# Kernel tuning notes

Measured on AMD Instinct MI355X. Metric: run time of the kernel, lower is better.

The kernel has to match this reference:

```python
import jax, jax.numpy as jnp
import numpy as np

B, L, HID = 512, 128, 384
N_LABELS, N_SLOTS = 32, 128


def setup_inputs() -> dict:
    key = jax.random.key(0)
    ks = jax.random.split(key, 16)

    def g(k, shape, scale):
        return jax.random.normal(k, shape, dtype=jnp.float32) * scale

    sent_lens = jax.random.randint(ks[0], (B,), 1, L + 1)
    mask = (jnp.arange(L)[None, :] < sent_lens[:, None]).astype(jnp.float32)[..., None]
    # zero out padded token positions to mimic the ragged original
    H = g(ks[1], (B, L, HID), 1.0) * mask
    c_slot_cont = g(ks[2], (B, L, HID), 1.0) * mask
    c_inte = g(ks[3], (B, HID), 1.0)
    s = 1.0 / np.sqrt(HID)
    return {
        "H": H,
        "c_slot_cont": c_slot_cont,
        "c_inte": c_inte,
        "W0": g(ks[4], (HID, HID), s),
        "W1": g(ks[5], (HID, HID), s),
        "W2": g(ks[6], (HID, HID), s),
        "W3": g(ks[7], (HID, HID), s),
        "W4": g(ks[8], (HID, HID), s),
        "b4": g(ks[9], (HID,), s),
        "W5": g(ks[10], (HID, 1), s),
        "V_SF": g(ks[11], (HID, HID), s),
        "W_inte": g(ks[12], (HID, N_LABELS), s),
        "W_slot": g(ks[13], (2 * HID, N_SLOTS), s),
        "sent_lens": sent_lens,
        "iteration_num": 3,
    }


def reference(H, c_slot_cont, c_inte, W0, W1, W2, W3, W4, b4, W5, V_SF,
              W_inte, W_slot, sent_lens, iteration_num):
    Ld = H.shape[1]
    mask = jnp.arange(Ld)[None, :] < sent_lens[:, None]          # [B, L] bool
    maskf = mask[..., None].astype(H.dtype)                       # [B, L, 1]
    neg_inf = jnp.finfo(H.dtype).min

    def sf_fusion(x, y):
        # SF_FusionLayer (dropout off / eval); inner loop runs once since nth=2
        x0 = jnp.tanh(x)
        y0 = jnp.tanh(y)
        f = jax.nn.sigmoid(jnp.tanh(x0 @ W0 + y0 @ W1) @ W2)
        x2 = f * x0 + x
        y2 = (1.0 - f) * y0 + y
        return f * x2 + (1.0 - f) * y2

    def id_fusion(x, y):
        # ID_FusionLayer; softmax over token dim, masked per sentence
        x0 = jnp.tanh(x)
        y0 = jnp.tanh(y)
        rates = ((x @ W3 + y @ W4 + b4) @ W5)[..., 0]             # [B, L]
        rates = jnp.where(mask, rates, neg_inf)
        alphas = jax.nn.softmax(rates, axis=1)[..., None]         # [B, L, 1]
        x2 = alphas * x0 + x
        y2 = (1.0 - alphas) * y0 + y
        return alphas * x2 + (1.0 - alphas) * y2

    r_inte = c_inte                                               # [B, HID]
    r_slot = c_slot_cont
    for _ in range(iteration_num):
        f_slot = sf_fusion(c_slot_cont, r_inte[:, None, :])       # [B, L, HID]
        f_slot = jnp.sum((f_slot @ V_SF) * maskf, axis=1)         # [B, HID]
        r_slot = f_slot[:, None, :] * c_slot_cont                 # [B, L, HID]
        f_inte = jnp.sum(id_fusion(r_slot, H) * maskf, axis=1)    # [B, HID]
        r_inte = f_inte + c_inte

    intent_output = r_inte @ W_inte                               # [B, n_labels]
    slot_output = jnp.concatenate([H, r_slot], axis=-1) @ W_slot  # [B, L, n_slots]
    return intent_output, slot_output
```

## Files before the change

### kernel.cpp

```cpp
#include <hip/hip_runtime.h>
#include <math.h>

#define HID 384
#define SLEN 128
#define NB 512
#define MTOK (NB*SLEN)
#define NLAB 32
#define NSLOT 128
#define GPITCH 72

typedef _Float16 h8 __attribute__((ext_vector_type(8)));
typedef _Float16 h4v __attribute__((ext_vector_type(4)));
typedef __bf16   b8 __attribute__((ext_vector_type(8)));
typedef float    f4 __attribute__((ext_vector_type(4)));

__device__ __forceinline__ float sane(float x){
  return __builtin_isfinite(x) ? x : 0.f;
}
__device__ __forceinline__ float clampf(float x, float lo, float hi){
  return fminf(hi, fmaxf(lo, x));
}
__device__ __forceinline__ float fast_rcp(float x){
  return __builtin_amdgcn_rcpf(x);
}
__device__ __forceinline__ float fast_tanh(float x){
  x = clampf(x, -15.f, 15.f);
  float e = __expf(2.f * x);
  return (e - 1.f) * fast_rcp(e + 1.f);
}
__device__ __forceinline__ float sigmoid_c(float x){
  x = clampf(x, -60.f, 60.f);
  return fast_rcp(1.f + __expf(-x));
}
__device__ __forceinline__ void split16(float x, _Float16* h, _Float16* l){
  _Float16 hh = (_Float16)x; *h = hh; *l = (_Float16)(x - (float)hh);
}
__device__ __forceinline__ h8 ldh(const _Float16* p){ return *reinterpret_cast<const h8*>(p); }
__device__ __forceinline__ b8 ldb(const __bf16* p){ return *reinterpret_cast<const b8*>(p); }
__device__ __forceinline__ f4 mfma16h(h8 a, h8 b, f4 c){
  return __builtin_amdgcn_mfma_f32_16x16x32_f16(a, b, c, 0, 0, 0);
}
__device__ __forceinline__ f4 mfma16b(b8 a, b8 b, f4 c){
  return __builtin_amdgcn_mfma_f32_16x16x32_bf16(a, b, c, 0, 0, 0);
}
__device__ __forceinline__ void bar_lds(){
  asm volatile("s_waitcnt lgkmcnt(0)" ::: "memory");
  __builtin_amdgcn_s_barrier();
}


__global__ void k_lens(const int* __restrict__ raw, int* __restrict__ lensN){
  const int b = threadIdx.x;
  __shared__ int is64;
  if (b == 0) is64 = (raw[1] == 0) ? 1 : 0;
  __syncthreads();
  int v = is64 ? raw[2 * b] : raw[b];
  v = v < 0 ? 0 : (v > SLEN ? SLEN : v);
  lensN[b] = v;
}

__global__ void k_wsplit16(const float* __restrict__ in, _Float16* __restrict__ outh,
                           _Float16* __restrict__ outl, int R, int C){
  int idx = blockIdx.x * blockDim.x + threadIdx.x;
  if (idx < R * C){
    int r = idx / C, c = idx - r * C;
    float v = sane(in[idx]);
    _Float16 h = (_Float16)v;
    outh[(size_t)c * R + r] = h;
    outl[(size_t)c * R + r] = (_Float16)(v - (float)h);
  }
}

__global__ void k_wsplitbf(const float* __restrict__ in, __bf16* __restrict__ outh,
                           __bf16* __restrict__ outl, int R, int C){
  int idx = blockIdx.x * blockDim.x + threadIdx.x;
  if (idx < R * C){
    int r = idx / C, c = idx - r * C;
    float v = sane(in[idx]);
    __bf16 h = (__bf16)v;
    outh[(size_t)c * R + r] = h;
    outl[(size_t)c * R + r] = (__bf16)(v - (float)h);
  }
}

__global__ void k_transpose32(const float* __restrict__ in, float* __restrict__ out,
                              int R, int C){
  int idx = blockIdx.x * blockDim.x + threadIdx.x;
  if (idx < R * C){ int r = idx / C, c = idx - r * C; out[(size_t)c * R + r] = sane(in[idx]); }
}

__global__ void k_sanecopy(const float* __restrict__ in, float* __restrict__ out, int n){
  int i = blockIdx.x * blockDim.x + threadIdx.x;
  if (i < n) out[i] = sane(in[i]);
}

__global__ void k_w35(const float* __restrict__ W3, const float* __restrict__ W4,
                      const float* __restrict__ b4, const float* __restrict__ W5,
                      float* __restrict__ w35, float* __restrict__ w45, float* __restrict__ b45){
  __shared__ float w5s[HID];
  int t = threadIdx.x;
  w5s[t] = sane(W5[t]);
  __syncthreads();
  float s3 = 0.f, s4 = 0.f;
  for (int j = 0; j < HID; ++j){
    float w5 = w5s[j];
    s3 += sane(W3[(size_t)t * HID + j]) * w5;
    s4 += sane(W4[(size_t)t * HID + j]) * w5;
  }
  w35[t] = s3; w45[t] = s4;
  if (t == 0){
    float s = 0.f;
    for (int j = 0; j < HID; ++j) s += sane(b4[j]) * w5s[j];
    *b45 = s;
  }
}

__global__ void k_hy(const float* __restrict__ Hm, const float* __restrict__ w45,
                     const float* __restrict__ b45, float* __restrict__ hy){
  int wave = threadIdx.x >> 6, lane = threadIdx.x & 63;
  int tok = blockIdx.x * 4 + wave;
  const float* row = Hm + (size_t)tok * HID;
  float s = 0.f;
#pragma unroll
  for (int i = 0; i < 6; ++i){ int k = lane + 64 * i; s += sane(row[k]) * w45[k]; }
  for (int off = 32; off; off >>= 1) s += __shfl_down(s, off);
  if (lane == 0) hy[tok] = clampf(s + *b45, -1e30f, 1e30f);
}

template <int TANH, int SANE_IN>
__global__ void k_vecmat(const float* __restrict__ in, const float* __restrict__ W,
                         float* __restrict__ out, float* __restrict__ pre_store){
  const int b = blockIdx.x, t = threadIdx.x;
  __shared__ float v[HID];
  float x = in[(size_t)b * HID + t];
  if (SANE_IN) x = sane(x);
  if (pre_store) pre_store[(size_t)b * HID + t] = x;
  if (TANH) x = fast_tanh(x);
  v[t] = x;
  __syncthreads();
  float s = 0.f;
  for (int k = 0; k < HID; ++k) s += v[k] * W[(size_t)k * HID + t];
  out[(size_t)b * HID + t] = clampf(s, -1e30f, 1e30f);
}

__global__ void __launch_bounds__(512, 4) k_p0c(
    const float* __restrict__ Cs,
    const _Float16* __restrict__ Wth, const _Float16* __restrict__ Wtl,
    const int* __restrict__ lens,
    _Float16* __restrict__ P0h, _Float16* __restrict__ P0l){
  __shared__ _Float16 Ah[64*GPITCH], Al[64*GPITCH];
  const int t = threadIdx.x;
  const int wave = t >> 6, lane = t & 63, quad = lane >> 4, lr = lane & 15;
  const int bx = blockIdx.x;
  const int b = bx >> 1;
  const int len = lens[b];
  const int row0 = (bx & 1) * 64;
  if (row0 >= len) return;
  const int gr0 = bx * 64;
  const int srow = t >> 3;
  const int sk8 = (t & 7) << 3;
  const int col0 = wave * 48;
  const float* abase = Cs + (size_t)(gr0 + srow) * HID + sk8;
  f4 c0 = *(const f4*)(abase);
  f4 c1 = *(const f4*)(abase + 4);
  f4 acc[4][3] = {};
  for (int ks = 0; ks < 6; ++ks){
    const int kk = ks * 64;
    {
      h8 th, tl;
#pragma unroll
      for (int j = 0; j < 8; ++j){
        float x = fast_tanh(sane((j < 4) ? c0[j] : c1[j - 4]));
        _Float16 h = (_Float16)x;
        th[j] = h; tl[j] = (_Float16)(x - (float)h);
      }
      *(h8*)&Ah[srow * GPITCH + sk8] = th;
      *(h8*)&Al[srow * GPITCH + sk8] = tl;
    }
    if (ks < 5){
      c0 = *(const f4*)(abase + kk + 64);
      c1 = *(const f4*)(abase + kk + 68);
    }
    bar_lds();
#pragma unroll
    for (int c = 0; c < 2; ++c){
      const int ro = c * 32 + quad * 8;
      h8 amh[4], aml[4];
#pragma unroll
      for (int mi = 0; mi < 4; ++mi){
        const int r = (mi * 16 + lr) * GPITCH + ro;
        amh[mi] = *(const h8*)&Ah[r]; aml[mi] = *(const h8*)&Al[r];
      }
#pragma unroll
      for (int ni = 0; ni < 3; ++ni){
        const size_t rb = ((size_t)(col0 + ni * 16 + lr)) * HID + kk + ro;
        h8 bh = ldh(Wth + rb), bl = ldh(Wtl + rb);
#pragma unroll
        for (int mi = 0; mi < 4; ++mi){
          acc[mi][ni] = mfma16h(amh[mi], bh, acc[mi][ni]);
          acc[mi][ni] = mfma16h(amh[mi], bl, acc[mi][ni]);
          acc[mi][ni] = mfma16h(aml[mi], bh, acc[mi][ni]);
        }
      }
    }
    bar_lds();
  }
#pragma unroll
  for (int ni = 0; ni < 3; ++ni){
    const int col = col0 + ni * 16 + lr;
#pragma unroll
    for (int mi = 0; mi < 4; ++mi)
#pragma unroll
      for (int r = 0; r < 4; ++r){
        const int rl = row0 + mi * 16 + quad * 4 + r;
        if (rl < len){
          const size_t o = ((size_t)(b * SLEN + rl)) * HID + col;
          _Float16 h, l; split16(acc[mi][ni][r], &h, &l);
          P0h[o] = h; P0l[o] = l;
        }
      }
  }
}

template <int MI>
__device__ __forceinline__ void g2n_mfma(f4 (&acc)[8][3],
    const _Float16* Ah, const _Float16* Al,
    const _Float16* __restrict__ Wth, const _Float16* __restrict__ Wtl,
    int col0, int kk, int quad, int lr){
#pragma unroll
  for (int c = 0; c < 2; ++c){
    const int ro = c * 32 + quad * 8;
    h8 amh[MI], aml[MI];
#pragma unroll
    for (int mi = 0; mi < MI; ++mi){
      const int r = (mi * 16 + lr) * GPITCH + ro;
      amh[mi] = *(const h8*)&Ah[r]; aml[mi] = *(const h8*)&Al[r];
    }
#pragma unroll
    for (int ni = 0; ni < 3; ++ni){
      const size_t rb = ((size_t)(col0 + ni * 16 + lr)) * HID + kk + ro;
      h8 bh = ldh(Wth + rb), bl = ldh(Wtl + rb);
#pragma unroll
      for (int mi = 0; mi < MI; ++mi){
        acc[mi][ni] = mfma16h(amh[mi], bh, acc[mi][ni]);
        acc[mi][ni] = mfma16h(amh[mi], bl, acc[mi][ni]);
        acc[mi][ni] = mfma16h(aml[mi], bh, acc[mi][ni]);
      }
    }
  }
}

template <int MI>
__device__ __forceinline__ void g2n_epi(const f4 (&acc)[8][3],
    const float* __restrict__ rb, const float* __restrict__ Cs,
    float* __restrict__ S, int b, int gr0, int len, int col0, int quad, int lr){
#pragma unroll
  for (int ni = 0; ni < 3; ++ni){
    const int col = col0 + ni * 16 + lr;
    const float yv = rb[col];
    const float y0 = fast_tanh(yv);
    float csum = 0.f;
#pragma unroll
    for (int mi = 0; mi < MI; ++mi)
#pragma unroll
      for (int r = 0; r < 4; ++r){
        const int rl = mi * 16 + quad * 4 + r;
        const int grow = gr0 + rl;
        const float f = sigmoid_c(acc[mi][ni][r]);
        const float omf = 1.f - f;
        const float xv = sane(Cs[(size_t)grow * HID + col]);
        const float x0 = fast_tanh(xv);
        const float outv = f * f * x0 + f * xv + omf * omf * y0 + omf * yv;
        csum += (rl < len) ? outv : 0.f;
      }
    csum += __shfl_xor(csum, 16);
    csum += __shfl_xor(csum, 32);
    if (quad == 0) S[(size_t)b * HID + col] = csum;
  }
}

__global__ void __launch_bounds__(512, 2) k_g2n(
    const _Float16* __restrict__ P0h, const _Float16* __restrict__ P0l,
    const _Float16* __restrict__ Wth, const _Float16* __restrict__ Wtl,
    const float* __restrict__ yw1, const float* __restrict__ Cs,
    const float* __restrict__ r_inte,
    const int* __restrict__ lens, float* __restrict__ S){
  __shared__ _Float16 Ah[128*GPITCH], Al[128*GPITCH];
  __shared__ float ywS[HID];
  const int t = threadIdx.x;
  const int wave = t >> 6, lane = t & 63, quad = lane >> 4, lr = lane & 15;
  const int b = blockIdx.x;
  const int len = lens[b];
  const int gr0 = b * SLEN;
  const int srow = t >> 3;
  const int sk8 = (t & 7) << 3;
  const int col0 = wave * 48;
  const bool hi = (len > 64);
  if (t < HID) ywS[t] = yw1[(size_t)b * HID + t];
  __syncthreads();
  const _Float16* pb0 = P0h + (size_t)(gr0 + srow) * HID + sk8;
  const _Float16* lb0 = P0l + (size_t)(gr0 + srow) * HID + sk8;
  const _Float16* pb1 = pb0 + (size_t)64 * HID;
  const _Float16* lb1 = lb0 + (size_t)64 * HID;
  h8 ph0 = ldh(pb0), pl0 = ldh(lb0), ph1 = {}, pl1 = {};
  if (hi){ ph1 = ldh(pb1); pl1 = ldh(lb1); }
  f4 acc[8][3] = {};
  for (int ks = 0; ks < 6; ++ks){
    const int kk = ks * 64;
    {
      const f4 ywa = *(const f4*)&ywS[kk + sk8];
      const f4 ywb = *(const f4*)&ywS[kk + sk8 + 4];
      h8 th, tl;
#pragma unroll
      for (int j = 0; j < 8; ++j){
        const float yw = (j < 4) ? ywa[j] : ywb[j - 4];
        float x = fast_tanh((float)ph0[j] + (float)pl0[j] + yw);
        _Float16 h = (_Float16)x;
        th[j] = h; tl[j] = (_Float16)(x - (float)h);
      }
      *(h8*)&Ah[srow * GPITCH + sk8] = th;
      *(h8*)&Al[srow * GPITCH + sk8] = tl;
      if (hi){
        h8 th1, tl1;
#pragma unroll
        for (int j = 0; j < 8; ++j){
          const float yw = (j < 4) ? ywa[j] : ywb[j - 4];
          float x = fast_tanh((float)ph1[j] + (float)pl1[j] + yw);
          _Float16 h = (_Float16)x;
          th1[j] = h; tl1[j] = (_Float16)(x - (float)h);
        }
        *(h8*)&Ah[(64 + srow) * GPITCH + sk8] = th1;
        *(h8*)&Al[(64 + srow) * GPITCH + sk8] = tl1;
      }
    }
    if (ks < 5){
      ph0 = ldh(pb0 + kk + 64); pl0 = ldh(lb0 + kk + 64);
      if (hi){ ph1 = ldh(pb1 + kk + 64); pl1 = ldh(lb1 + kk + 64); }
    }
    bar_lds();
    if (hi) g2n_mfma<8>(acc, Ah, Al, Wth, Wtl, col0, kk, quad, lr);
    else    g2n_mfma<4>(acc, Ah, Al, Wth, Wtl, col0, kk, quad, lr);
    bar_lds();
  }
  const float* rb = r_inte + (size_t)b * HID;
  if (hi) g2n_epi<8>(acc, rb, Cs, S, b, gr0, len, col0, quad, lr);
  else    g2n_epi<4>(acc, rb, Cs, S, b, gr0, len, col0, quad, lr);
}

__global__ void k_stageD2(
    const float* __restrict__ Cs, const float* __restrict__ Hm,
    const float* __restrict__ ci, const float* __restrict__ Vsc,
    const float* __restrict__ W1c, const float* __restrict__ w35,
    const float* __restrict__ hy, const int* __restrict__ lens,
    const float* __restrict__ S, float* __restrict__ fss_g,
    float* __restrict__ r_inte, float* __restrict__ yw1){
  const int b = blockIdx.x;
  const int t = threadIdx.x;
  const int len = lens[b];
  __shared__ float Sl[HID], fssS[HID], fssw[HID], tri[HID];
  __shared__ float rates[SLEN];
  __shared__ float wA[SLEN], wB[SLEN], wC[SLEN], wD[SLEN];
  Sl[t] = S[(size_t)b * HID + t];
  __syncthreads();
  {
    float s = 0.f;
    for (int k = 0; k < HID; ++k) s += Sl[k] * Vsc[(size_t)k * HID + t];
    const float fs = clampf(s, -1e30f, 1e30f);
    fssS[t] = fs; fssw[t] = fs * w35[t];
    fss_g[(size_t)b * HID + t] = fs;
  }
  __syncthreads();
  const int wave = t >> 6, lane = t & 63;
  for (int l = wave; l < SLEN; l += 6){
    const float* row = Cs + ((size_t)b * SLEN + l) * HID;
    float s = 0.f;
#pragma unroll
    for (int i = 0; i < 6; ++i){ int k = lane + 64 * i; s += sane(row[k]) * fssw[k]; }
    for (int off = 32; off; off >>= 1) s += __shfl_down(s, off);
    if (lane == 0) rates[l] = clampf(s + hy[(size_t)b * SLEN + l], -1e30f, 1e30f);
  }
  __syncthreads();
  if (wave == 0){
    float r0 = (lane < len) ? rates[lane] : -3.0e38f;
    float r1 = (lane + 64 < len) ? rates[lane + 64] : -3.0e38f;
    float mx = fmaxf(r0, r1);
    for (int off = 32; off; off >>= 1) mx = fmaxf(mx, __shfl_xor(mx, off));
    float e0 = (lane < len) ? __expf(r0 - mx) : 0.f;
    float e1 = (lane + 64 < len) ? __expf(r1 - mx) : 0.f;
    float sm = e0 + e1;
    for (int off = 32; off; off >>= 1) sm += __shfl_xor(sm, off);
    const float inv = (sm > 0.f) ? (1.f / sm) : 0.f;
    float a0 = clampf(e0 * inv, 0.f, 1.f), a1 = clampf(e1 * inv, 0.f, 1.f);
    wA[lane] = a0 * a0; wB[lane] = a0;
    wC[lane] = (1.f - a0) * (1.f - a0); wD[lane] = 1.f - a0;
    wA[lane + 64] = a1 * a1; wB[lane + 64] = a1;
    wC[lane + 64] = (1.f - a1) * (1.f - a1); wD[lane + 64] = 1.f - a1;
  }
  __syncthreads();
  {
    const float fs = fssS[t];
    float acc = 0.f;
#pragma unroll 4
    for (int l = 0; l < len; ++l){
      const float cv = sane(Cs[((size_t)b * SLEN + l) * HID + t]);
      const float hv = sane(Hm[((size_t)b * SLEN + l) * HID + t]);
      const float rs = fs * cv;
      acc += wA[l] * fast_tanh(rs) + wB[l] * rs + wC[l] * fast_tanh(hv) + wD[l] * hv;
    }
    const float ri = clampf(acc + sane(ci[(size_t)b * HID + t]), -1e30f, 1e30f);
    r_inte[(size_t)b * HID + t] = ri;
    tri[t] = fast_tanh(ri);
  }
  __syncthreads();
  {
    float s = 0.f;
    for (int k = 0; k < HID; ++k) s += tri[k] * W1c[(size_t)k * HID + t];
    yw1[(size_t)b * HID + t] = clampf(s, -1e30f, 1e30f);
  }
}

__global__ void k_intent(const float* __restrict__ r_inte, const float* __restrict__ Wit,
                         float* __restrict__ out){
  const int t = threadIdx.x;
  const int b = blockIdx.x * 4 + (t >> 5);
  const int n = t & 31;
  const float* wr = Wit + (size_t)n * HID;
  const float* rr = r_inte + (size_t)b * HID;
  float s = 0.f;
  for (int k = 0; k < HID; ++k) s += rr[k] * wr[k];
  out[(size_t)b * NLAB + n] = clampf(s, -3e38f, 3e38f);
}

__global__ void __launch_bounds__(256, 2) k_slot_bf(
    const float* __restrict__ Hm, const float* __restrict__ Cs,
    const float* __restrict__ fss, const int* __restrict__ lens,
    const __bf16* __restrict__ Wth, const __bf16* __restrict__ Wtl,
    float* __restrict__ out){
  const int wave = threadIdx.x >> 6, lane = threadIdx.x & 63;
  const int quad = lane >> 4, lr = lane & 15;
  const int m0 = blockIdx.x * 128 + (wave & 1) * 64;
  const int n0 = (wave >> 1) * 64;
  const int b = blockIdx.x;
  const int ko = quad * 8;
  const int len = lens[b];
  if ((wave & 1) * 64 >= len){
#pragma unroll
    for (int mi = 0; mi < 4; ++mi)
#pragma unroll
      for (int ni = 0; ni < 4; ++ni)
#pragma unroll
        for (int r = 0; r < 4; ++r){
          const int row = m0 + mi * 16 + quad * 4 + r;
          const int col = n0 + ni * 16 + lr;
          out[(size_t)row * NSLOT + col] = 0.f;
        }
    return;
  }
  f4 acc[4][4] = {};
  for (int kk = 0; kk < 2 * HID; kk += 32){
    b8 ah[4], al[4], bh[4], bl[4];
#pragma unroll
    for (int i = 0; i < 4; ++i){
      size_t rb = (size_t)(n0 + i * 16 + lr) * (2 * HID) + kk + ko;
      bh[i] = ldb(Wth + rb); bl[i] = ldb(Wtl + rb);
    }
    if (kk < HID){
#pragma unroll
      for (int i = 0; i < 4; ++i){
        const float* hrow = Hm + (size_t)(m0 + i * 16 + lr) * HID + kk + ko;
        b8 vh, vl;
#pragma unroll
        for (int j = 0; j < 8; ++j){
          float v = sane(hrow[j]);
          __bf16 h = (__bf16)v;
          vh[j] = h; vl[j] = (__bf16)(v - (float)h);
        }
        ah[i] = vh; al[i] = vl;
      }
    } else {
      const int k2 = kk - HID + ko;
      float fv[8];
#pragma unroll
      for (int j = 0; j < 8; ++j) fv[j] = fss[(size_t)b * HID + k2 + j];
#pragma unroll
      for (int i = 0; i < 4; ++i){
        const float* crow = Cs + (size_t)(m0 + i * 16 + lr) * HID + k2;
        b8 vh, vl;
#pragma unroll
        for (int j = 0; j < 8; ++j){
          float v = fv[j] * sane(crow[j]);
          __bf16 h = (__bf16)v;
          vh[j] = h; vl[j] = (__bf16)(v - (float)h);
        }
        ah[i] = vh; al[i] = vl;
      }
    }
#pragma unroll
    for (int mi = 0; mi < 4; ++mi)
#pragma unroll
      for (int ni = 0; ni < 4; ++ni){
        acc[mi][ni] = mfma16b(ah[mi], bh[ni], acc[mi][ni]);
        acc[mi][ni] = mfma16b(ah[mi], bl[ni], acc[mi][ni]);
        acc[mi][ni] = mfma16b(al[mi], bh[ni], acc[mi][ni]);
      }
  }
#pragma unroll
  for (int mi = 0; mi < 4; ++mi)
#pragma unroll
    for (int ni = 0; ni < 4; ++ni)
#pragma unroll
      for (int r = 0; r < 4; ++r){
        const int row = m0 + mi * 16 + quad * 4 + r;
        const int col = n0 + ni * 16 + lr;
        out[(size_t)row * NSLOT + col] = clampf(acc[mi][ni][r], -3e38f, 3e38f);
      }
}

extern "C" void kernel_launch(void* const* d_in, const int* in_sizes, int n_in,
                              void* d_out, int out_size, void* d_ws, size_t ws_size,
                              hipStream_t stream){
  (void)in_sizes; (void)n_in; (void)out_size;
  const float* Hm  = (const float*)d_in[0];
  const float* Cs  = (const float*)d_in[1];
  const float* ci  = (const float*)d_in[2];
  const float* W0  = (const float*)d_in[3];
  const float* W1  = (const float*)d_in[4];
  const float* W2  = (const float*)d_in[5];
  const float* W3  = (const float*)d_in[6];
  const float* W4  = (const float*)d_in[7];
  const float* b4  = (const float*)d_in[8];
  const float* W5  = (const float*)d_in[9];
  const float* Vs  = (const float*)d_in[10];
  const float* Wi  = (const float*)d_in[11];
  const float* Wsl = (const float*)d_in[12];
  const int* lens_raw = (const int*)d_in[13];

  char* base = (char*)d_ws;
  size_t off = 0;
  auto alloc = [&](size_t bytes) -> void* {
    void* p = base + off; off += (bytes + 255) & ~(size_t)255; return p;
  };
  const size_t NT = (size_t)MTOK * HID;
  _Float16* P0h  = (_Float16*)alloc(NT * 2);
  _Float16* P0l  = (_Float16*)alloc(NT * 2);
  _Float16* W0th = (_Float16*)alloc((size_t)HID * HID * 2);
  _Float16* W0tl = (_Float16*)alloc((size_t)HID * HID * 2);
  _Float16* W2th = (_Float16*)alloc((size_t)HID * HID * 2);
  _Float16* W2tl = (_Float16*)alloc((size_t)HID * HID * 2);
  __bf16*   Wsth = (__bf16*)alloc((size_t)2 * HID * NSLOT * 2);
  __bf16*   Wstl = (__bf16*)alloc((size_t)2 * HID * NSLOT * 2);
  float* W1c    = (float*)alloc((size_t)HID * HID * 4);
  float* Vsc    = (float*)alloc((size_t)HID * HID * 4);
  float* Wit    = (float*)alloc((size_t)HID * NLAB * 4);
  float* w35    = (float*)alloc(HID * 4);
  float* w45    = (float*)alloc(HID * 4);
  float* b45    = (float*)alloc(4);
  float* hy     = (float*)alloc((size_t)MTOK * 4);
  float* yw1    = (float*)alloc((size_t)NB * HID * 4);
  float* r_inte = (float*)alloc((size_t)NB * HID * 4);
  float* S      = (float*)alloc((size_t)NB * HID * 4);
  float* fss    = (float*)alloc((size_t)NB * HID * 4);
  int* lensN    = (int*)alloc((size_t)NB * 4);
  if (off > ws_size) return;

  k_lens<<<1, NB, 0, stream>>>(lens_raw, lensN);
  k_wsplit16<<<(HID * HID + 255) / 256, 256, 0, stream>>>(W0, W0th, W0tl, HID, HID);
  k_wsplit16<<<(HID * HID + 255) / 256, 256, 0, stream>>>(W2, W2th, W2tl, HID, HID);
  k_wsplitbf<<<(2 * HID * NSLOT + 255) / 256, 256, 0, stream>>>(Wsl, Wsth, Wstl, 2 * HID, NSLOT);
  k_sanecopy<<<(HID * HID + 255) / 256, 256, 0, stream>>>(W1, W1c, HID * HID);
  k_sanecopy<<<(HID * HID + 255) / 256, 256, 0, stream>>>(Vs, Vsc, HID * HID);
  k_transpose32<<<(HID * NLAB + 255) / 256, 256, 0, stream>>>(Wi, Wit, HID, NLAB);
  k_w35<<<1, HID, 0, stream>>>(W3, W4, b4, W5, w35, w45, b45);
  k_hy<<<MTOK / 4, 256, 0, stream>>>(Hm, w45, b45, hy);
  k_p0c<<<MTOK / 64, 512, 0, stream>>>(Cs, W0th, W0tl, lensN, P0h, P0l);

  k_vecmat<1, 1><<<NB, HID, 0, stream>>>(ci, W1c, yw1, r_inte);

  for (int it = 0; it < 3; ++it){
    k_g2n<<<NB, 512, 0, stream>>>(P0h, P0l, W2th, W2tl, yw1, Cs, r_inte, lensN, S);
    k_stageD2<<<NB, HID, 0, stream>>>(Cs, Hm, ci, Vsc, W1c, w35, hy, lensN,
                                      S, fss, r_inte, yw1);
  }

  float* outp = (float*)d_out;
  k_intent<<<NB / 4, 128, 0, stream>>>(r_inte, Wit, outp);
  k_slot_bf<<<NB, 256, 0, stream>>>(Hm, Cs, fss, lensN, Wsth, Wstl, outp + (size_t)NB * NLAB);
}
```

Baseline: 997.2 us.

## Double-buffer LDS staging in GEMM kernels and skip padded tokens

Converts the k_p0c and k_g2n MFMA loops to double-buffered LDS tiles. The next K-slice is staged (tanh and hi/lo split) while MFMAs run on the current slice, which removes one barrier per iteration. The k_g2n body is templated on MI, so the len>64 branch is resolved once instead of per iteration. k_hy and the rates loop in k_stageD2 now skip tokens beyond each sentence length. This doubles LDS use, which may lower occupancy, especially in k_g2n.

```diff
diff --git a/kernel.cpp b/kernel.cpp
--- a/kernel.cpp
+++ b/kernel.cpp
@@ -116,9 +116,12 @@
 }
 
 __global__ void k_hy(const float* __restrict__ Hm, const float* __restrict__ w45,
-                     const float* __restrict__ b45, float* __restrict__ hy){
+                     const float* __restrict__ b45, const int* __restrict__ lens,
+                     float* __restrict__ hy){
   int wave = threadIdx.x >> 6, lane = threadIdx.x & 63;
   int tok = blockIdx.x * 4 + wave;
+  const int b = tok >> 7, l = tok & (SLEN - 1);
+  if (l >= lens[b]) return;
   const float* row = Hm + (size_t)tok * HID;
   float s = 0.f;
 #pragma unroll
@@ -143,12 +146,40 @@
   out[(size_t)b * HID + t] = clampf(s, -1e30f, 1e30f);
 }
 
+template <int MI>
+__device__ __forceinline__ void mfma_phase(f4 (&acc)[MI][3],
+    const _Float16* Ah, const _Float16* Al,
+    const _Float16* __restrict__ Wth, const _Float16* __restrict__ Wtl,
+    int col0, int kk, int quad, int lr){
+#pragma unroll
+  for (int c = 0; c < 2; ++c){
+    const int ro = c * 32 + quad * 8;
+    h8 amh[MI], aml[MI];
+#pragma unroll
+    for (int mi = 0; mi < MI; ++mi){
+      const int r = (mi * 16 + lr) * GPITCH + ro;
+      amh[mi] = *(const h8*)&Ah[r]; aml[mi] = *(const h8*)&Al[r];
+    }
+#pragma unroll
+    for (int ni = 0; ni < 3; ++ni){
+      const size_t rb = ((size_t)(col0 + ni * 16 + lr)) * HID + kk + ro;
+      h8 bh = ldh(Wth + rb), bl = ldh(Wtl + rb);
+#pragma unroll
+      for (int mi = 0; mi < MI; ++mi){
+        acc[mi][ni] = mfma16h(amh[mi], bh, acc[mi][ni]);
+        acc[mi][ni] = mfma16h(amh[mi], bl, acc[mi][ni]);
+        acc[mi][ni] = mfma16h(aml[mi], bh, acc[mi][ni]);
+      }
+    }
+  }
+}
+
 __global__ void __launch_bounds__(512, 4) k_p0c(
     const float* __restrict__ Cs,
     const _Float16* __restrict__ Wth, const _Float16* __restrict__ Wtl,
     const int* __restrict__ lens,
     _Float16* __restrict__ P0h, _Float16* __restrict__ P0l){
-  __shared__ _Float16 Ah[64*GPITCH], Al[64*GPITCH];
+  __shared__ _Float16 Ah[2][64*GPITCH], Al[2][64*GPITCH];
   const int t = threadIdx.x;
   const int wave = t >> 6, lane = t & 63, quad = lane >> 4, lr = lane & 15;
   const int bx = blockIdx.x;
@@ -161,48 +192,34 @@
   const int sk8 = (t & 7) << 3;
   const int col0 = wave * 48;
   const float* abase = Cs + (size_t)(gr0 + srow) * HID + sk8;
-  f4 c0 = *(const f4*)(abase);
-  f4 c1 = *(const f4*)(abase + 4);
+
+  auto stage = [&](int buf, f4 c0, f4 c1){
+    h8 th, tl;
+#pragma unroll
+    for (int j = 0; j < 8; ++j){
+      float x = fast_tanh(sane((j < 4) ? c0[j] : c1[j - 4]));
+      _Float16 h = (_Float16)x;
+      th[j] = h; tl[j] = (_Float16)(x - (float)h);
+    }
+    *(h8*)&Ah[buf][srow * GPITCH + sk8] = th;
+    *(h8*)&Al[buf][srow * GPITCH + sk8] = tl;
+  };
+
   f4 acc[4][3] = {};
+  f4 c0 = *(const f4*)(abase), c1 = *(const f4*)(abase + 4);
+  stage(0, c0, c1);
+  c0 = *(const f4*)(abase + 64); c1 = *(const f4*)(abase + 68);
+  bar_lds();
   for (int ks = 0; ks < 6; ++ks){
-    const int kk = ks * 64;
-    {
-      h8 th, tl;
-#pragma unroll
-      for (int j = 0; j < 8; ++j){
-        float x = fast_tanh(sane((j < 4) ? c0[j] : c1[j - 4]));
-        _Float16 h = (_Float16)x;
-        th[j] = h; tl[j] = (_Float16)(x - (float)h);
-      }
-      *(h8*)&Ah[srow * GPITCH + sk8] = th;
-      *(h8*)&Al[srow * GPITCH + sk8] = tl;
-    }
+    const int cur = ks & 1;
     if (ks < 5){
-      c0 = *(const f4*)(abase + kk + 64);
-      c1 = *(const f4*)(abase + kk + 68);
-    }
-    bar_lds();
-#pragma unroll
-    for (int c = 0; c < 2; ++c){
-      const int ro = c * 32 + quad * 8;
-      h8 amh[4], aml[4];
-#pragma unroll
-      for (int mi = 0; mi < 4; ++mi){
-        const int r = (mi * 16 + lr) * GPITCH + ro;
-        amh[mi] = *(const h8*)&Ah[r]; aml[mi] = *(const h8*)&Al[r];
-      }
-#pragma unroll
-      for (int ni = 0; ni < 3; ++ni){
-        const size_t rb = ((size_t)(col0 + ni * 16 + lr)) * HID + kk + ro;
-        h8 bh = ldh(Wth + rb), bl = ldh(Wtl + rb);
-#pragma unroll
-        for (int mi = 0; mi < 4; ++mi){
-          acc[mi][ni] = mfma16h(amh[mi], bh, acc[mi][ni]);
-          acc[mi][ni] = mfma16h(amh[mi], bl, acc[mi][ni]);
-          acc[mi][ni] = mfma16h(aml[mi], bh, acc[mi][ni]);
-        }
-      }
-    }
+      stage(cur ^ 1, c0, c1);
+      if (ks < 4){
+        c0 = *(const f4*)(abase + (ks + 2) * 64);
+        c1 = *(const f4*)(abase + (ks + 2) * 64 + 4);
+      }
+    }
+    mfma_phase<4>(acc, &Ah[cur][0], &Al[cur][0], Wth, Wtl, col0, ks * 64, quad, lr);
     bar_lds();
   }
 #pragma unroll
@@ -223,35 +240,7 @@
 }
 
 template <int MI>
-__device__ __forceinline__ void g2n_mfma(f4 (&acc)[8][3],
-    const _Float16* Ah, const _Float16* Al,
-    const _Float16* __restrict__ Wth, const _Float16* __restrict__ Wtl,
-    int col0, int kk, int quad, int lr){
-#pragma unroll
-  for (int c = 0; c < 2; ++c){
-    const int ro = c * 32 + quad * 8;
-    h8 amh[MI], aml[MI];
-#pragma unroll
-    for (int mi = 0; mi < MI; ++mi){
-      const int r = (mi * 16 + lr) * GPITCH + ro;
-      amh[mi] = *(const h8*)&Ah[r]; aml[mi] = *(const h8*)&Al[r];
-    }
-#pragma unroll
-    for (int ni = 0; ni < 3; ++ni){
-      const size_t rb = ((size_t)(col0 + ni * 16 + lr)) * HID + kk + ro;
-      h8 bh = ldh(Wth + rb), bl = ldh(Wtl + rb);
-#pragma unroll
-      for (int mi = 0; mi < MI; ++mi){
-        acc[mi][ni] = mfma16h(amh[mi], bh, acc[mi][ni]);
-        acc[mi][ni] = mfma16h(amh[mi], bl, acc[mi][ni]);
-        acc[mi][ni] = mfma16h(aml[mi], bh, acc[mi][ni]);
-      }
-    }
-  }
-}
-
-template <int MI>
-__device__ __forceinline__ void g2n_epi(const f4 (&acc)[8][3],
+__device__ __forceinline__ void g2n_epi(const f4 (&acc)[MI][3],
     const float* __restrict__ rb, const float* __restrict__ Cs,
     float* __restrict__ S, int b, int gr0, int len, int col0, int quad, int lr){
 #pragma unroll
@@ -279,72 +268,94 @@
   }
 }
 
+template <int MI>
+__device__ __forceinline__ void g2n_core(
+    _Float16 (&Ah)[2][128*GPITCH], _Float16 (&Al)[2][128*GPITCH],
+    const float* ywS,
+    const _Float16* __restrict__ P0h, const _Float16* __restrict__ P0l,
+    const _Float16* __restrict__ Wth, const _Float16* __restrict__ Wtl,
+    const float* __restrict__ Cs, const float* __restrict__ r_inte,
+    float* __restrict__ S, int b, int len,
+    int srow, int sk8, int col0, int quad, int lr){
+  const int gr0 = b * SLEN;
+  const _Float16* pb0 = P0h + (size_t)(gr0 + srow) * HID + sk8;
+  const _Float16* lb0 = P0l + (size_t)(gr0 + srow) * HID + sk8;
+  const _Float16* pb1 = pb0 + (size_t)64 * HID;
+  const _Float16* lb1 = lb0 + (size_t)64 * HID;
+
+  h8 ph0, pl0, ph1 = {}, pl1 = {};
+  auto loadp = [&](int kk){
+    ph0 = ldh(pb0 + kk); pl0 = ldh(lb0 + kk);
+    if (MI == 8){ ph1 = ldh(pb1 + kk); pl1 = ldh(lb1 + kk); }
+  };
+  auto stage = [&](int buf, int kk){
+    const f4 ywa = *(const f4*)&ywS[kk + sk8];
+    const f4 ywb = *(const f4*)&ywS[kk + sk8 + 4];
+    h8 th, tl;
+#pragma unroll
+    for (int j = 0; j < 8; ++j){
+      const float yw = (j < 4) ? ywa[j] : ywb[j - 4];
+      float x = fast_tanh((float)ph0[j] + (float)pl0[j] + yw);
+      _Float16 h = (_Float16)x;
+      th[j] = h; tl[j] = (_Float16)(x - (float)h);
+    }
+    *(h8*)&Ah[buf][srow * GPITCH + sk8] = th;
+    *(h8*)&Al[buf][srow * GPITCH + sk8] = tl;
+    if (MI == 8){
+      h8 th1, tl1;
+#pragma unroll
+      for (int j = 0; j < 8; ++j){
+        const float yw = (j < 4) ? ywa[j] : ywb[j - 4];
+        float x = fast_tanh((float)ph1[j] + (float)pl1[j] + yw);
+        _Float16 h = (_Float16)x;
+        th1[j] = h; tl1[j] = (_Float16)(x - (float)h);
+      }
+      *(h8*)&Ah[buf][(64 + srow) * GPITCH + sk8] = th1;
+      *(h8*)&Al[buf][(64 + srow) * GPITCH + sk8] = tl1;
+    }
+  };
+
+  f4 acc[MI][3] = {};
+  loadp(0);
+  stage(0, 0);
+  loadp(64);
+  bar_lds();
+  for (int ks = 0; ks < 6; ++ks){
+    const int cur = ks & 1;
+    if (ks < 5){
+      stage(cur ^ 1, (ks + 1) * 64);
+      if (ks < 4) loadp((ks + 2) * 64);
+    }
+    mfma_phase<MI>(acc, &Ah[cur][0], &Al[cur][0], Wth, Wtl, col0, ks * 64, quad, lr);
+    bar_lds();
+  }
+  const float* rb = r_inte + (size_t)b * HID;
+  g2n_epi<MI>(acc, rb, Cs, S, b, gr0, len, col0, quad, lr);
+}
+
 __global__ void __launch_bounds__(512, 2) k_g2n(
     const _Float16* __restrict__ P0h, const _Float16* __restrict__ P0l,
     const _Float16* __restrict__ Wth, const _Float16* __restrict__ Wtl,
     const float* __restrict__ yw1, const float* __restrict__ Cs,
     const float* __restrict__ r_inte,
     const int* __restrict__ lens, float* __restrict__ S){
-  __shared__ _Float16 Ah[128*GPITCH], Al[128*GPITCH];
+  __shared__ _Float16 Ah[2][128*GPITCH], Al[2][128*GPITCH];
   __shared__ float ywS[HID];
   const int t = threadIdx.x;
   const int wave = t >> 6, lane = t & 63, quad = lane >> 4, lr = lane & 15;
   const int b = blockIdx.x;
   const int len = lens[b];
-  const int gr0 = b * SLEN;
   const int srow = t >> 3;
   const int sk8 = (t & 7) << 3;
   const int col0 = wave * 48;
-  const bool hi = (len > 64);
   if (t < HID) ywS[t] = yw1[(size_t)b * HID + t];
-  __syncthreads();
-  const _Float16* pb0 = P0h + (size_t)(gr0 + srow) * HID + sk8;
-  const _Float16* lb0 = P0l + (size_t)(gr0 + srow) * HID + sk8;
-  const _Float16* pb1 = pb0 + (size_t)64 * HID;
-  const _Float16* lb1 = lb0 + (size_t)64 * HID;
-  h8 ph0 = ldh(pb0), pl0 = ldh(lb0), ph1 = {}, pl1 = {};
-  if (hi){ ph1 = ldh(pb1); pl1 = ldh(lb1); }
-  f4 acc[8][3] = {};
-  for (int ks = 0; ks < 6; ++ks){
-    const int kk = ks * 64;
-    {
-      const f4 ywa = *(const f4*)&ywS[kk + sk8];
-      const f4 ywb = *(const f4*)&ywS[kk + sk8 + 4];
-      h8 th, tl;
-#pragma unroll
-      for (int j = 0; j < 8; ++j){
-        const float yw = (j < 4) ? ywa[j] : ywb[j - 4];
-        float x = fast_tanh((float)ph0[j] + (float)pl0[j] + yw);
-        _Float16 h = (_Float16)x;
-        th[j] = h; tl[j] = (_Float16)(x - (float)h);
-      }
-      *(h8*)&Ah[srow * GPITCH + sk8] = th;
-      *(h8*)&Al[srow * GPITCH + sk8] = tl;
-      if (hi){
-        h8 th1, tl1;
-#pragma unroll
-        for (int j = 0; j < 8; ++j){
-          const float yw = (j < 4) ? ywa[j] : ywb[j - 4];
-          float x = fast_tanh((float)ph1[j] + (float)pl1[j] + yw);
-          _Float16 h = (_Float16)x;
-          th1[j] = h; tl1[j] = (_Float16)(x - (float)h);
-        }
-        *(h8*)&Ah[(64 + srow) * GPITCH + sk8] = th1;
-        *(h8*)&Al[(64 + srow) * GPITCH + sk8] = tl1;
-      }
-    }
-    if (ks < 5){
-      ph0 = ldh(pb0 + kk + 64); pl0 = ldh(lb0 + kk + 64);
-      if (hi){ ph1 = ldh(pb1 + kk + 64); pl1 = ldh(lb1 + kk + 64); }
-    }
-    bar_lds();
-    if (hi) g2n_mfma<8>(acc, Ah, Al, Wth, Wtl, col0, kk, quad, lr);
-    else    g2n_mfma<4>(acc, Ah, Al, Wth, Wtl, col0, kk, quad, lr);
-    bar_lds();
-  }
-  const float* rb = r_inte + (size_t)b * HID;
-  if (hi) g2n_epi<8>(acc, rb, Cs, S, b, gr0, len, col0, quad, lr);
-  else    g2n_epi<4>(acc, rb, Cs, S, b, gr0, len, col0, quad, lr);
+  bar_lds();
+  if (len > 64)
+    g2n_core<8>(Ah, Al, ywS, P0h, P0l, Wth, Wtl, Cs, r_inte, S, b, len,
+                srow, sk8, col0, quad, lr);
+  else
+    g2n_core<4>(Ah, Al, ywS, P0h, P0l, Wth, Wtl, Cs, r_inte, S, b, len,
+                srow, sk8, col0, quad, lr);
 }
 
 __global__ void k_stageD2(
@@ -371,7 +382,7 @@
   }
   __syncthreads();
   const int wave = t >> 6, lane = t & 63;
-  for (int l = wave; l < SLEN; l += 6){
+  for (int l = wave; l < len; l += 6){
     const float* row = Cs + ((size_t)b * SLEN + l) * HID;
     float s = 0.f;
 #pragma unroll
@@ -571,7 +582,7 @@
   k_sanecopy<<<(HID * HID + 255) / 256, 256, 0, stream>>>(Vs, Vsc, HID * HID);
   k_transpose32<<<(HID * NLAB + 255) / 256, 256, 0, stream>>>(Wi, Wit, HID, NLAB);
   k_w35<<<1, HID, 0, stream>>>(W3, W4, b4, W5, w35, w45, b45);
-  k_hy<<<MTOK / 4, 256, 0, stream>>>(Hm, w45, b45, hy);
+  k_hy<<<MTOK / 4, 256, 0, stream>>>(Hm, w45, b45, lensN, hy);
   k_p0c<<<MTOK / 64, 512, 0, stream>>>(Cs, W0th, W0tl, lensN, P0h, P0l);
 
   k_vecmat<1, 1><<<NB, HID, 0, stream>>>(ci, W1c, yw1, r_inte);
```

Result: faster. 970.7 us (-2.7%).
